# Performance work log

Hardware: AMD Instinct MI355X
Metric: run time of the kernel (lower is better)

The kernel has to match this reference:

```python
import jax, jax.numpy as jnp
import numpy as np

N = 50000
IN_DIM = 256
HID = 64
HEADS = 4
OUT_DIM = 64
E = 800000
SLOPE = 0.2


def gat_conv(x, src, dst, W, a_src, a_dst, bias, heads, out_ch):
    """PyG-style GATConv: gather -> edge attention -> segment softmax -> scatter.
    x: [N, in], W: [in, heads*out_ch], a_src/a_dst: [heads, out_ch], bias: [heads*out_ch].
    Returns [N, heads*out_ch] (heads concatenated)."""
    n = x.shape[0]
    h = (x @ W).reshape(n, heads, out_ch)               # [N, H, C]
    s = jnp.einsum('nhc,hc->nh', h, a_src)              # [N, H]
    d = jnp.einsum('nhc,hc->nh', h, a_dst)              # [N, H]
    e = jax.nn.leaky_relu(s[src] + d[dst], SLOPE)       # [E, H]
    emax = jax.ops.segment_max(e, dst, num_segments=n)  # stable softmax per dst
    ex = jnp.exp(e - emax[dst])
    denom = jax.ops.segment_sum(ex, dst, num_segments=n)
    alpha = ex / (denom[dst] + 1e-16)                   # [E, H]
    msg = h[src] * alpha[:, :, None]                    # [E, H, C]
    out = jax.ops.segment_sum(msg, dst, num_segments=n) # [N, H, C]
    return out.reshape(n, heads * out_ch) + bias


def setup_inputs() -> dict:
    key = jax.random.key(0)
    ks = jax.random.split(key, 12)
    x = jax.random.normal(ks[0], (N, IN_DIM), dtype=jnp.float32)
    edge_index = jax.random.randint(ks[1], (2, E), 0, N, dtype=jnp.int64)
    sc = 0.1
    params = {
        'W1': jax.random.normal(ks[2], (IN_DIM, HEADS * HID), dtype=jnp.float32) * sc,
        'a_src1': jax.random.normal(ks[3], (HEADS, HID), dtype=jnp.float32) * sc,
        'a_dst1': jax.random.normal(ks[4], (HEADS, HID), dtype=jnp.float32) * sc,
        'b1': jnp.zeros((HEADS * HID,), dtype=jnp.float32),
        'W2': jax.random.normal(ks[5], (HEADS * HID, HID), dtype=jnp.float32) * sc,
        'a_src2': jax.random.normal(ks[6], (1, HID), dtype=jnp.float32) * sc,
        'a_dst2': jax.random.normal(ks[7], (1, HID), dtype=jnp.float32) * sc,
        'b2': jnp.zeros((HID,), dtype=jnp.float32),
        'Wf1': jax.random.normal(ks[8], (HID, HID), dtype=jnp.float32) * sc,
        'bf1': jnp.zeros((HID,), dtype=jnp.float32),
        'Wf2': jax.random.normal(ks[9], (HID, OUT_DIM), dtype=jnp.float32) * sc,
        'bf2': jnp.zeros((OUT_DIM,), dtype=jnp.float32),
    }
    return {'x': x, 'edge_index': edge_index, **params}


def reference(x, edge_index, W1, a_src1, a_dst1, b1, W2, a_src2, a_dst2, b2,
              Wf1, bf1, Wf2, bf2):
    n = x.shape[0]
    # PyG GATConv adds self-loops by default
    loops = jnp.arange(n, dtype=edge_index.dtype)
    src = jnp.concatenate([edge_index[0], loops])
    dst = jnp.concatenate([edge_index[1], loops])
    h = jax.nn.relu(gat_conv(x, src, dst, W1, a_src1, a_dst1, b1, HEADS, HID))
    h = jax.nn.relu(gat_conv(h, src, dst, W2, a_src2, a_dst2, b2, 1, HID))
    h = jax.nn.relu(h @ Wf1 + bf1)
    return jax.nn.softmax(h @ Wf2 + bf2, axis=1)
```

## Files before the change

### kernel.cpp

```cpp
#include <hip/hip_runtime.h>

#define NNODES 50000
#define NEDGES 800000
#define INDIM  256
#define HIDC   64
#define HEADS  4
static constexpr int ETOT = NEDGES + NNODES;

typedef _Float16 half4 __attribute__((ext_vector_type(4)));
typedef _Float16 half8 __attribute__((ext_vector_type(8)));
typedef short    s16x8 __attribute__((ext_vector_type(8)));
typedef short    s16x4 __attribute__((ext_vector_type(4)));
typedef float    f32x4 __attribute__((ext_vector_type(4)));

__device__ __forceinline__ unsigned short f2bf(float f) {
    unsigned u = __float_as_uint(f);
    u += 0x7fffu + ((u >> 16) & 1u);
    return (unsigned short)(u >> 16);
}
__device__ __forceinline__ float bf2f(unsigned short h) {
    return __uint_as_float(((unsigned)h) << 16);
}

__global__ void detect_k(const unsigned* __restrict__ ei32, int* __restrict__ flag) {
    __shared__ int any32;
    if (threadIdx.x == 0) any32 = 0;
    __syncthreads();
    if (ei32[1 + 2 * threadIdx.x] != 0u) any32 = 1;
    __syncthreads();
    if (threadIdx.x == 0) *flag = !any32;
}

__device__ __forceinline__ int load_idx(const void* ei, int is64, size_t pos) {
    return is64 ? (int)((const long long*)ei)[pos] : ((const int*)ei)[pos];
}

__global__ __launch_bounds__(256)
void hist_k(const void* __restrict__ ei, const int* __restrict__ flag,
            int* __restrict__ count) {
    int e = blockIdx.x * 256 + threadIdx.x;
    if (e >= ETOT) return;
    int is64 = *flag;
    int dst = (e < NEDGES) ? load_idx(ei, is64, (size_t)NEDGES + e) : (e - NEDGES);
    atomicAdd(&count[dst], 1);
}

__global__ __launch_bounds__(1024)
void scan1_k(const int* __restrict__ count, int* __restrict__ rowptr,
             int* __restrict__ bsum, int n) {
    __shared__ int wsum[16];
    const int tid = threadIdx.x;
    const int lane = tid & 63;
    const int w = tid >> 6;
    int i = blockIdx.x * 1024 + tid;
    int v = (i < n) ? count[i] : 0;
    int x = v;
    #pragma unroll
    for (int dd = 1; dd < 64; dd <<= 1) {
        int y = __shfl_up(x, dd);
        if (lane >= dd) x += y;
    }
    if (lane == 63) wsum[w] = x;
    __syncthreads();
    int woff = 0, total = 0;
    #pragma unroll
    for (int j = 0; j < 16; ++j) {
        if (j < w) woff += wsum[j];
        total += wsum[j];
    }
    if (i < n) rowptr[i] = woff + x - v;
    if (tid == 0) bsum[blockIdx.x] = total;
}

__global__ void scan2_k(int* __restrict__ bsum, int* __restrict__ bpre, int nb,
                        int* __restrict__ rowptr, int n) {
    int lane = threadIdx.x;
    int v = (lane < nb) ? bsum[lane] : 0;
    int x = v;
    #pragma unroll
    for (int dd = 1; dd < 64; dd <<= 1) {
        int y = __shfl_up(x, dd);
        if (lane >= dd) x += y;
    }
    if (lane < nb) bpre[lane] = x - v;
    if (lane == 63) rowptr[n] = x;
}

__global__ __launch_bounds__(1024)
void scan3_k(int* __restrict__ rowptr, const int* __restrict__ bpre, int n) {
    int i = blockIdx.x * 1024 + threadIdx.x;
    if (i < n) rowptr[i] += bpre[blockIdx.x];
}

__global__ __launch_bounds__(256)
void scatter_k(const void* __restrict__ ei, const int* __restrict__ flag,
               const int* __restrict__ rowptr, int* __restrict__ fill,
               int* __restrict__ csr_src) {
    int e = blockIdx.x * 256 + threadIdx.x;
    if (e >= ETOT) return;
    int is64 = *flag;
    int src, dst;
    if (e < NEDGES) {
        src = load_idx(ei, is64, (size_t)e);
        dst = load_idx(ei, is64, (size_t)NEDGES + e);
    } else {
        src = e - NEDGES; dst = src;
    }
    int pos = rowptr[dst] + atomicAdd(&fill[dst], 1);
    csr_src[pos] = src;
}

__global__ __launch_bounds__(256)
void convw_k(const float* __restrict__ W, unsigned short* __restrict__ t_hi,
             unsigned short* __restrict__ t_lo, int K, int N) {
    int idx = blockIdx.x * 256 + threadIdx.x;
    if (idx >= K * N) return;
    int k = idx / N, n = idx % N;
    float w = W[idx];
    unsigned short hi = f2bf(w);
    unsigned short lo = f2bf(w - bf2f(hi));
    t_hi[(size_t)n * K + k] = hi;
    t_lo[(size_t)n * K + k] = lo;
}

template<int BN, int SD>
__global__ __launch_bounds__(256)
void gemm_mfma_k(const float* __restrict__ A,
                 const unsigned short* __restrict__ Bt_hi,
                 const unsigned short* __restrict__ Bt_lo,
                 float* __restrict__ C, _Float16* __restrict__ Ch,
                 const float* __restrict__ asrc, const float* __restrict__ adst,
                 float* __restrict__ S, float* __restrict__ D,
                 int M, int N, int K) {
    constexpr int CB = BN / 32;
    constexpr int BI = (BN * 4) / 256;
    __shared__ unsigned short sAh[128][40], sAl[128][40];
    __shared__ unsigned short sBh[BN][40], sBl[BN][40];
    const int tid = threadIdx.x;
    const int bm = blockIdx.y * 128;
    const int bn = blockIdx.x * BN;
    const int w = tid >> 6, lane = tid & 63;
    const int wr = w >> 1, wc = w & 1;
    const int lr = lane & 15, lk = lane >> 4;

    f32x4 acc[4][CB] = {};

    for (int k0 = 0; k0 < K; k0 += 32) {
        float4 av[4];
        #pragma unroll
        for (int i = 0; i < 4; ++i) {
            int idx = tid + 256 * i;
            int row = idx >> 3, c4 = idx & 7;
            int grow = bm + row; if (grow >= M) grow = M - 1;
            av[i] = *(const float4*)(A + (size_t)grow * K + k0 + c4 * 4);
        }
        s16x8 bhv[BI], blv[BI];
        #pragma unroll
        for (int i = 0; i < BI; ++i) {
            int idx = tid + 256 * i;
            int col = idx >> 2, ch = idx & 3;
            bhv[i] = *(const s16x8*)(Bt_hi + (size_t)(bn + col) * K + k0 + ch * 8);
            blv[i] = *(const s16x8*)(Bt_lo + (size_t)(bn + col) * K + k0 + ch * 8);
        }
        __syncthreads();
        #pragma unroll
        for (int i = 0; i < 4; ++i) {
            int idx = tid + 256 * i;
            int row = idx >> 3, c4 = idx & 7;
            float vs[4] = {av[i].x, av[i].y, av[i].z, av[i].w};
            unsigned short h[4], l[4];
            #pragma unroll
            for (int j = 0; j < 4; ++j) {
                h[j] = f2bf(vs[j]);
                l[j] = f2bf(vs[j] - bf2f(h[j]));
            }
            *(s16x4*)&sAh[row][c4 * 4] = (s16x4){(short)h[0], (short)h[1], (short)h[2], (short)h[3]};
            *(s16x4*)&sAl[row][c4 * 4] = (s16x4){(short)l[0], (short)l[1], (short)l[2], (short)l[3]};
        }
        #pragma unroll
        for (int i = 0; i < BI; ++i) {
            int idx = tid + 256 * i;
            int col = idx >> 2, ch = idx & 3;
            *(s16x8*)&sBh[col][ch * 8] = bhv[i];
            *(s16x8*)&sBl[col][ch * 8] = blv[i];
        }
        __syncthreads();
        s16x8 afh[4], afl[4], bfh[CB], bfl[CB];
        #pragma unroll
        for (int rb = 0; rb < 4; ++rb) {
            int row = wr * 64 + rb * 16 + lr;
            afh[rb] = *(const s16x8*)&sAh[row][lk * 8];
            afl[rb] = *(const s16x8*)&sAl[row][lk * 8];
        }
        #pragma unroll
        for (int cb = 0; cb < CB; ++cb) {
            int col = wc * (BN / 2) + cb * 16 + lr;
            bfh[cb] = *(const s16x8*)&sBh[col][lk * 8];
            bfl[cb] = *(const s16x8*)&sBl[col][lk * 8];
        }
        #pragma unroll
        for (int rb = 0; rb < 4; ++rb)
            #pragma unroll
            for (int cb = 0; cb < CB; ++cb) {
                acc[rb][cb] = __builtin_amdgcn_mfma_f32_16x16x32_bf16(afh[rb], bfh[cb], acc[rb][cb], 0, 0, 0);
                acc[rb][cb] = __builtin_amdgcn_mfma_f32_16x16x32_bf16(afh[rb], bfl[cb], acc[rb][cb], 0, 0, 0);
                acc[rb][cb] = __builtin_amdgcn_mfma_f32_16x16x32_bf16(afl[rb], bfh[cb], acc[rb][cb], 0, 0, 0);
            }
    }
    #pragma unroll
    for (int rb = 0; rb < 4; ++rb)
        #pragma unroll
        for (int cb = 0; cb < CB; ++cb)
            #pragma unroll
            for (int r = 0; r < 4; ++r) {
                int row = bm + wr * 64 + rb * 16 + lk * 4 + r;
                int col = bn + wc * (BN / 2) + cb * 16 + lr;
                if (row < M) {
                    float v = acc[rb][cb][r];
                    if constexpr (SD == 0) C[(size_t)row * N + col] = v;
                    if (Ch) Ch[(size_t)row * N + col] = (_Float16)v;
                }
            }
    if constexpr (SD != 0) {
        float af[CB], df[CB];
        #pragma unroll
        for (int cb = 0; cb < CB; ++cb) {
            int colg = bn + wc * (BN / 2) + cb * 16 + lr;
            af[cb] = asrc[colg];
            df[cb] = adst[colg];
        }
        #pragma unroll
        for (int rb = 0; rb < 4; ++rb)
            #pragma unroll
            for (int r = 0; r < 4; ++r) {
                float ps = 0.f, pd = 0.f;
                #pragma unroll
                for (int cb = 0; cb < CB; ++cb) {
                    ps += acc[rb][cb][r] * af[cb];
                    pd += acc[rb][cb][r] * df[cb];
                }
                #pragma unroll
                for (int m = 1; m < 16; m <<= 1) {
                    ps += __shfl_xor(ps, m);
                    pd += __shfl_xor(pd, m);
                }
                int row = bm + wr * 64 + rb * 16 + lk * 4 + r;
                if (lr == 0 && row < M) {
                    if constexpr (SD == 1) {
                        int head = (bn + wc * (BN / 2)) >> 6;
                        S[(size_t)row * (N >> 6) + head] = ps;
                        D[(size_t)row * (N >> 6) + head] = pd;
                    } else {
                        atomicAdd(&S[row], ps);
                        atomicAdd(&D[row], pd);
                    }
                }
            }
    }
}

template<int H>
__global__ __launch_bounds__(256)
void sd_k(const float* __restrict__ hfeat, const float* __restrict__ a_src,
          const float* __restrict__ a_dst, float* __restrict__ s,
          float* __restrict__ d, int n) {
    const int lane = threadIdx.x & 63;
    const int node = blockIdx.x * 4 + (threadIdx.x >> 6);
    if (node >= n) return;
    const float* row = hfeat + (size_t)node * (H * 64);
    #pragma unroll
    for (int h = 0; h < H; ++h) {
        float f = row[h * 64 + lane];
        float vs = f * a_src[h * 64 + lane];
        float vd = f * a_dst[h * 64 + lane];
        #pragma unroll
        for (int m = 32; m; m >>= 1) {
            vs += __shfl_xor(vs, m);
            vd += __shfl_xor(vd, m);
        }
        if (lane == 0) { s[node * H + h] = vs; d[node * H + h] = vd; }
    }
}

__device__ __forceinline__ float leaky(float e) { return (e > 0.f) ? e : 0.2f * e; }

__device__ __forceinline__ float sel4(const float v[4], int idx) {
    float r = v[0];
    r = (idx == 1) ? v[1] : r;
    r = (idx == 2) ? v[2] : r;
    r = (idx == 3) ? v[3] : r;
    return r;
}

__device__ __forceinline__ void osm_upd(float& m, float& sm, float e) {
    float nm = fmaxf(m, e);
    sm = sm * __expf(m - nm) + __expf(e - nm);
    m = nm;
}

template<int H, bool EB>
__global__ __launch_bounds__(256)
void agg_k(const float* __restrict__ hfeat, const _Float16* __restrict__ hhalf,
           const float* __restrict__ s, const float* __restrict__ d,
           const float* __restrict__ bias, const int* __restrict__ rowptr,
           const int* __restrict__ csr_src, float* __restrict__ ebuf,
           float* __restrict__ out, int n) {
    const int lane = threadIdx.x & 63;
    const int node = blockIdx.x * 4 + (threadIdx.x >> 6);
    if (node >= n) return;
    const int beg = rowptr[node];
    const int end = rowptr[node + 1];
    float dh[H], dn[H], inv[H];
    #pragma unroll
    for (int h = 0; h < H; ++h) {
        dh[h] = d[node * H + h];
        dn[h] = 0.f;
    }

    if constexpr (EB) {
        for (int i = beg + lane; i < end; i += 64) {
            int sidx = csr_src[i];
            if constexpr (H == 4) {
                float4 sv = *(const float4*)(s + (size_t)sidx * 4);
                float4 ex;
                ex.x = __expf(leaky(sv.x + dh[0]));
                ex.y = __expf(leaky(sv.y + dh[1]));
                ex.z = __expf(leaky(sv.z + dh[2]));
                ex.w = __expf(leaky(sv.w + dh[3]));
                *(float4*)(ebuf + (size_t)i * 4) = ex;
                dn[0] += ex.x; dn[1] += ex.y; dn[2] += ex.z; dn[3] += ex.w;
            } else {
                float ex = __expf(leaky(s[sidx] + dh[0]));
                ebuf[i] = ex;
                dn[0] += ex;
            }
        }
        #pragma unroll
        for (int h = 0; h < H; ++h) {
            #pragma unroll
            for (int m = 32; m; m >>= 1) dn[h] += __shfl_xor(dn[h], m);
            inv[h] = 1.f / (dn[h] + 1e-16f);
        }

        if constexpr (H == 4) {
            const half8* H8 = (const half8*)hhalf;
            const int sub = lane >> 5;
            const int c8 = lane & 31;
            const int head = c8 >> 3;
            const float invh = sel4(inv, head);
            float acc[8] = {};
            int i = beg;
            for (; i + 7 < end; i += 8) {
                int e0 = i + sub, e1 = i + 2 + sub, e2 = i + 4 + sub, e3 = i + 6 + sub;
                int s0 = csr_src[e0], s1 = csr_src[e1];
                int s2 = csr_src[e2], s3 = csr_src[e3];
                float x0 = ebuf[(size_t)e0 * 4 + head];
                float x1 = ebuf[(size_t)e1 * 4 + head];
                float x2 = ebuf[(size_t)e2 * 4 + head];
                float x3 = ebuf[(size_t)e3 * 4 + head];
                half8 h0 = H8[(size_t)s0 * 32 + c8];
                half8 h1 = H8[(size_t)s1 * 32 + c8];
                half8 h2 = H8[(size_t)s2 * 32 + c8];
                half8 h3 = H8[(size_t)s3 * 32 + c8];
                #pragma unroll
                for (int j = 0; j < 8; ++j)
                    acc[j] += x0 * (float)h0[j] + x1 * (float)h1[j]
                            + x2 * (float)h2[j] + x3 * (float)h3[j];
            }
            for (; i < end; i += 2) {
                int e = i + sub;
                if (e < end) {
                    int s0 = csr_src[e];
                    float x = ebuf[(size_t)e * 4 + head];
                    half8 hh = H8[(size_t)s0 * 32 + c8];
                    #pragma unroll
                    for (int j = 0; j < 8; ++j) acc[j] += x * (float)hh[j];
                }
            }
            #pragma unroll
            for (int j = 0; j < 8; ++j) acc[j] += __shfl_xor(acc[j], 32);
            if (lane < 32) {
                float4 b0 = *(const float4*)(bias + c8 * 8);
                float4 b1 = *(const float4*)(bias + c8 * 8 + 4);
                float4 o0, o1;
                o0.x = fmaxf(acc[0] * invh + b0.x, 0.f);
                o0.y = fmaxf(acc[1] * invh + b0.y, 0.f);
                o0.z = fmaxf(acc[2] * invh + b0.z, 0.f);
                o0.w = fmaxf(acc[3] * invh + b0.w, 0.f);
                o1.x = fmaxf(acc[4] * invh + b1.x, 0.f);
                o1.y = fmaxf(acc[5] * invh + b1.y, 0.f);
                o1.z = fmaxf(acc[6] * invh + b1.z, 0.f);
                o1.w = fmaxf(acc[7] * invh + b1.w, 0.f);
                *(float4*)(out + (size_t)node * 256 + c8 * 8) = o0;
                *(float4*)(out + (size_t)node * 256 + c8 * 8 + 4) = o1;
            }
        } else {
            const half8* H8 = (const half8*)hhalf;
            const int sub = lane >> 3;
            const int c8 = lane & 7;
            float acc[8] = {};
            int i = beg;
            for (; i + 15 < end; i += 16) {
                int e0 = i + sub, e1 = i + 8 + sub;
                int s0 = csr_src[e0], s1 = csr_src[e1];
                float x0 = ebuf[e0], x1 = ebuf[e1];
                half8 h0 = H8[(size_t)s0 * 8 + c8];
                half8 h1 = H8[(size_t)s1 * 8 + c8];
                #pragma unroll
                for (int j = 0; j < 8; ++j)
                    acc[j] += x0 * (float)h0[j] + x1 * (float)h1[j];
            }
            for (; i < end; i += 8) {
                int e = i + sub;
                if (e < end) {
                    int s0 = csr_src[e];
                    float x = ebuf[e];
                    half8 hh = H8[(size_t)s0 * 8 + c8];
                    #pragma unroll
                    for (int j = 0; j < 8; ++j) acc[j] += x * (float)hh[j];
                }
            }
            #pragma unroll
            for (int m = 8; m <= 32; m <<= 1)
                #pragma unroll
                for (int j = 0; j < 8; ++j) acc[j] += __shfl_xor(acc[j], m);
            if (lane < 8) {
                float4 b0 = *(const float4*)(bias + c8 * 8);
                float4 b1 = *(const float4*)(bias + c8 * 8 + 4);
                float4 o0, o1;
                o0.x = fmaxf(acc[0] * inv[0] + b0.x, 0.f);
                o0.y = fmaxf(acc[1] * inv[0] + b0.y, 0.f);
                o0.z = fmaxf(acc[2] * inv[0] + b0.z, 0.f);
                o0.w = fmaxf(acc[3] * inv[0] + b0.w, 0.f);
                o1.x = fmaxf(acc[4] * inv[0] + b1.x, 0.f);
                o1.y = fmaxf(acc[5] * inv[0] + b1.y, 0.f);
                o1.z = fmaxf(acc[6] * inv[0] + b1.z, 0.f);
                o1.w = fmaxf(acc[7] * inv[0] + b1.w, 0.f);
                *(float4*)(out + (size_t)node * 64 + c8 * 8) = o0;
                *(float4*)(out + (size_t)node * 64 + c8 * 8 + 4) = o1;
            }
        }
    } else {
        float mx[H], sm[H];
        #pragma unroll
        for (int h = 0; h < H; ++h) { mx[h] = -3.0e38f; sm[h] = 0.f; }
        for (int i = beg + lane; i < end; i += 64) {
            int sidx = csr_src[i];
            if constexpr (H == 4) {
                float4 sv = *(const float4*)(s + (size_t)sidx * 4);
                osm_upd(mx[0], sm[0], leaky(sv.x + dh[0]));
                osm_upd(mx[1], sm[1], leaky(sv.y + dh[1]));
                osm_upd(mx[2], sm[2], leaky(sv.z + dh[2]));
                osm_upd(mx[3], sm[3], leaky(sv.w + dh[3]));
            } else {
                osm_upd(mx[0], sm[0], leaky(s[sidx] + dh[0]));
            }
        }
        #pragma unroll
        for (int h = 0; h < H; ++h) {
            #pragma unroll
            for (int dd = 32; dd; dd >>= 1) {
                float om = __shfl_xor(mx[h], dd);
                float os = __shfl_xor(sm[h], dd);
                float nm = fmaxf(mx[h], om);
                sm[h] = sm[h] * __expf(mx[h] - nm) + os * __expf(om - nm);
                mx[h] = nm;
            }
            inv[h] = 1.f / (sm[h] + 1e-16f);
        }
        if constexpr (H == 4) {
            const int head = lane >> 4;
            const float invh = sel4(inv, head);
            const float mxh = sel4(mx, head);
            const float dhh = sel4(dh, head);
            const float4* H4 = (const float4*)hfeat;
            float4 acc = {0.f, 0.f, 0.f, 0.f};
            for (int i = beg; i < end; ++i) {
                int s0 = csr_src[i];
                float al0 = __expf(leaky(s[(size_t)s0 * 4 + head] + dhh) - mxh) * invh;
                float4 h0 = H4[(size_t)s0 * 64 + lane];
                acc.x += al0 * h0.x; acc.y += al0 * h0.y;
                acc.z += al0 * h0.z; acc.w += al0 * h0.w;
            }
            float4 bv = ((const float4*)bias)[lane];
            float4 o;
            o.x = fmaxf(acc.x + bv.x, 0.f); o.y = fmaxf(acc.y + bv.y, 0.f);
            o.z = fmaxf(acc.z + bv.z, 0.f); o.w = fmaxf(acc.w + bv.w, 0.f);
            ((float4*)out)[(size_t)node * 64 + lane] = o;
        } else {
            float acc = 0.f;
            for (int i = beg; i < end; ++i) {
                int s0 = csr_src[i];
                float a0 = __expf(leaky(s[s0] + dh[0]) - mx[0]) * inv[0];
                acc += a0 * hfeat[(size_t)s0 * 64 + lane];
            }
            float v = acc + bias[lane];
            out[(size_t)node * 64 + lane] = fmaxf(v, 0.f);
        }
    }
}

__global__ __launch_bounds__(256)
void ff_k(const float* __restrict__ in, const float* __restrict__ Wf1,
          const float* __restrict__ bf1, const float* __restrict__ Wf2,
          const float* __restrict__ bf2, float* __restrict__ out, int n) {
    __shared__ float w1[64 * 64];
    __shared__ float w2[64 * 64];
    __shared__ float xrow[4][64];
    __shared__ float yrow[4][64];
    const int tid = threadIdx.x;
    for (int i = tid; i < 64 * 64; i += 256) { w1[i] = Wf1[i]; w2[i] = Wf2[i]; }
    __syncthreads();
    const int wv = tid >> 6;
    const int lane = tid & 63;
    const float B1 = bf1[lane], B2 = bf2[lane];
    const int nblk = (n + 3) / 4;
    for (int nb = blockIdx.x; nb < nblk; nb += gridDim.x) {
        int node = nb * 4 + wv;
        int nd = node < n ? node : (n - 1);
        float x = in[(size_t)nd * 64 + lane];
        xrow[wv][lane] = x;
        float y = B1;
        #pragma unroll 8
        for (int k = 0; k < 64; ++k) y += xrow[wv][k] * w1[k * 64 + lane];
        y = fmaxf(y, 0.f);
        yrow[wv][lane] = y;
        float z = B2;
        #pragma unroll 8
        for (int k = 0; k < 64; ++k) z += yrow[wv][k] * w2[k * 64 + lane];
        float m = z;
        #pragma unroll
        for (int dd = 32; dd; dd >>= 1) m = fmaxf(m, __shfl_xor(m, dd));
        float ex = __expf(z - m);
        float sum = ex;
        #pragma unroll
        for (int dd = 32; dd; dd >>= 1) sum += __shfl_xor(sum, dd);
        if (node < n) out[(size_t)node * 64 + lane] = ex / sum;
    }
}

extern "C" void kernel_launch(void* const* d_in, const int* in_sizes, int n_in,
                              void* d_out, int out_size, void* d_ws, size_t ws_size,
                              hipStream_t stream) {
    const float* x      = (const float*)d_in[0];
    const void*  ei     = d_in[1];
    const float* W1     = (const float*)d_in[2];
    const float* a_src1 = (const float*)d_in[3];
    const float* a_dst1 = (const float*)d_in[4];
    const float* b1     = (const float*)d_in[5];
    const float* W2     = (const float*)d_in[6];
    const float* a_src2 = (const float*)d_in[7];
    const float* a_dst2 = (const float*)d_in[8];
    const float* b2     = (const float*)d_in[9];
    const float* Wf1    = (const float*)d_in[10];
    const float* bf1    = (const float*)d_in[11];
    const float* Wf2    = (const float*)d_in[12];
    const float* bf2    = (const float*)d_in[13];
    float* outp = (float*)d_out;

    char* ws = (char*)d_ws;
    size_t off = 0;
    auto take = [&](size_t bytes) -> char* {
        char* p = ws + off;
        off += (bytes + 255) & ~(size_t)255;
        return p;
    };
    int*   flag   = (int*)take(4);
    int*   count  = (int*)take((size_t)NNODES * 4);
    int*   fill   = (int*)take((size_t)NNODES * 4);
    int*   rowptr = (int*)take((size_t)(NNODES + 1) * 4);
    int*   bsum   = (int*)take(64 * 4);
    int*   bpre   = (int*)take(64 * 4);
    int*   csr    = (int*)take((size_t)ETOT * 4);
    unsigned short* w1t_hi = (unsigned short*)take((size_t)256 * 256 * 2);
    unsigned short* w1t_lo = (unsigned short*)take((size_t)256 * 256 * 2);
    unsigned short* w2t_hi = (unsigned short*)take((size_t)64 * 256 * 2);
    unsigned short* w2t_lo = (unsigned short*)take((size_t)64 * 256 * 2);
    float* h1     = (float*)take((size_t)NNODES * 256 * 4);
    float* agg1   = (float*)take((size_t)NNODES * 256 * 4);
    float* s1     = (float*)take((size_t)NNODES * HEADS * 4);
    float* d1     = (float*)take((size_t)NNODES * HEADS * 4);
    float* ebuf   = (float*)take((size_t)ETOT * HEADS * 4);
    _Float16* h1h = (_Float16*)take((size_t)NNODES * 256 * 2);
    const bool eb_ok = (off <= ws_size);
    float*    h2   = h1;
    float*    s2   = s1;
    float*    d2   = d1;
    float*    agg2 = agg1;
    _Float16* h2h  = h1h;

    detect_k<<<1, 128, 0, stream>>>((const unsigned*)ei, flag);
    hipMemsetAsync(count, 0, (size_t)NNODES * 4, stream);
    hipMemsetAsync(fill, 0, (size_t)NNODES * 4, stream);
    const int eblocks = (ETOT + 255) / 256;
    hist_k<<<eblocks, 256, 0, stream>>>(ei, flag, count);
    const int sblocks = (NNODES + 1023) / 1024;
    scan1_k<<<sblocks, 1024, 0, stream>>>(count, rowptr, bsum, NNODES);
    scan2_k<<<1, 64, 0, stream>>>(bsum, bpre, sblocks, rowptr, NNODES);
    scan3_k<<<sblocks, 1024, 0, stream>>>(rowptr, bpre, NNODES);
    scatter_k<<<eblocks, 256, 0, stream>>>(ei, flag, rowptr, fill, csr);

    convw_k<<<(256 * 256) / 256, 256, 0, stream>>>(W1, w1t_hi, w1t_lo, 256, 256);
    convw_k<<<(256 * 64) / 256, 256, 0, stream>>>(W2, w2t_hi, w2t_lo, 256, 64);

    const int nodeblocks = NNODES / 4;
    const int mblocks = (NNODES + 127) / 128;
    const dim3 gg1(2, mblocks);
    const dim3 gg2(1, mblocks);

    if (eb_ok) {
        gemm_mfma_k<128, 1><<<gg1, 256, 0, stream>>>(x, w1t_hi, w1t_lo,
            nullptr, h1h, a_src1, a_dst1, s1, d1, NNODES, 256, 256);
        agg_k<HEADS, true><<<nodeblocks, 256, 0, stream>>>(h1, h1h, s1, d1, b1,
            rowptr, csr, ebuf, agg1, NNODES);

        hipMemsetAsync(s2, 0, (size_t)NNODES * 4, stream);
        hipMemsetAsync(d2, 0, (size_t)NNODES * 4, stream);
        gemm_mfma_k<64, 2><<<gg2, 256, 0, stream>>>(agg1, w2t_hi, w2t_lo,
            nullptr, h2h, a_src2, a_dst2, s2, d2, NNODES, 64, 256);
        agg_k<1, true><<<nodeblocks, 256, 0, stream>>>(h2, h2h, s2, d2, b2,
            rowptr, csr, ebuf, agg2, NNODES);
    } else {
        gemm_mfma_k<128, 0><<<gg1, 256, 0, stream>>>(x, w1t_hi, w1t_lo,
            h1, nullptr, nullptr, nullptr, nullptr, nullptr, NNODES, 256, 256);
        sd_k<HEADS><<<nodeblocks, 256, 0, stream>>>(h1, a_src1, a_dst1, s1, d1, NNODES);
        agg_k<HEADS, false><<<nodeblocks, 256, 0, stream>>>(h1, h1h, s1, d1, b1,
            rowptr, csr, ebuf, agg1, NNODES);
        gemm_mfma_k<64, 0><<<gg2, 256, 0, stream>>>(agg1, w2t_hi, w2t_lo,
            h2, nullptr, nullptr, nullptr, nullptr, nullptr, NNODES, 64, 256);
        sd_k<1><<<nodeblocks, 256, 0, stream>>>(h2, a_src2, a_dst2, s2, d2, NNODES);
        agg_k<1, false><<<nodeblocks, 256, 0, stream>>>(h2, h2h, s2, d2, b2,
            rowptr, csr, ebuf, agg2, NNODES);
    }

    ff_k<<<1024, 256, 0, stream>>>(agg2, Wf1, bf1, Wf2, bf2, outp, NNODES);
}
```

Measured before the change: 323.0 us.

## Split layer-1 aggregation into per-head passes over head-major fp16 features

```diff
diff --git a/kernel.cpp b/kernel.cpp
--- a/kernel.cpp
+++ b/kernel.cpp
@@ -123,7 +123,7 @@
     t_lo[(size_t)n * K + k] = lo;
 }
 
-template<int BN, int SD>
+template<int BN, int SD, bool HM>
 __global__ __launch_bounds__(256)
 void gemm_mfma_k(const float* __restrict__ A,
                  const unsigned short* __restrict__ Bt_hi,
@@ -218,7 +218,12 @@
                 if (row < M) {
                     float v = acc[rb][cb][r];
                     if constexpr (SD == 0) C[(size_t)row * N + col] = v;
-                    if (Ch) Ch[(size_t)row * N + col] = (_Float16)v;
+                    if (Ch) {
+                        size_t cidx = HM
+                            ? ((size_t)(col >> 6) * M + row) * 64 + (col & 63)
+                            : (size_t)row * N + col;
+                        Ch[cidx] = (_Float16)v;
+                    }
                 }
             }
     if constexpr (SD != 0) {
@@ -296,6 +301,100 @@
     float nm = fmaxf(m, e);
     sm = sm * __expf(m - nm) + __expf(e - nm);
     m = nm;
+}
+
+__global__ __launch_bounds__(256)
+void pass1_k(const float* __restrict__ s, const float* __restrict__ d,
+             const int* __restrict__ rowptr, const int* __restrict__ csr_src,
+             float* __restrict__ ebuf, float* __restrict__ invv, int n) {
+    const int lane = threadIdx.x & 63;
+    const int node = blockIdx.x * 4 + (threadIdx.x >> 6);
+    if (node >= n) return;
+    const int beg = rowptr[node];
+    const int end = rowptr[node + 1];
+    float4 dh = ((const float4*)d)[node];
+    float dn0 = 0.f, dn1 = 0.f, dn2 = 0.f, dn3 = 0.f;
+    for (int i = beg + lane; i < end; i += 64) {
+        int sidx = csr_src[i];
+        float4 sv = ((const float4*)s)[sidx];
+        float e0 = __expf(leaky(sv.x + dh.x));
+        float e1 = __expf(leaky(sv.y + dh.y));
+        float e2 = __expf(leaky(sv.z + dh.z));
+        float e3 = __expf(leaky(sv.w + dh.w));
+        ebuf[i] = e0;
+        ebuf[(size_t)ETOT + i] = e1;
+        ebuf[(size_t)2 * ETOT + i] = e2;
+        ebuf[(size_t)3 * ETOT + i] = e3;
+        dn0 += e0; dn1 += e1; dn2 += e2; dn3 += e3;
+    }
+    #pragma unroll
+    for (int m = 32; m; m >>= 1) {
+        dn0 += __shfl_xor(dn0, m); dn1 += __shfl_xor(dn1, m);
+        dn2 += __shfl_xor(dn2, m); dn3 += __shfl_xor(dn3, m);
+    }
+    if (lane == 0) {
+        float4 iv;
+        iv.x = 1.f / (dn0 + 1e-16f); iv.y = 1.f / (dn1 + 1e-16f);
+        iv.z = 1.f / (dn2 + 1e-16f); iv.w = 1.f / (dn3 + 1e-16f);
+        ((float4*)invv)[node] = iv;
+    }
+}
+
+__global__ __launch_bounds__(256)
+void agg3_k(const _Float16* __restrict__ hh, const float* __restrict__ exh,
+            const float* __restrict__ invv, const float* __restrict__ bias,
+            const int* __restrict__ rowptr, const int* __restrict__ csr_src,
+            float* __restrict__ out, int head, int n) {
+    const int lane = threadIdx.x & 63;
+    const int node = blockIdx.x * 4 + (threadIdx.x >> 6);
+    if (node >= n) return;
+    const int beg = rowptr[node];
+    const int end = rowptr[node + 1];
+    const half8* H8 = (const half8*)hh;
+    const int sub = lane >> 3;
+    const int c8 = lane & 7;
+    float acc[8] = {};
+    int i = beg;
+    for (; i + 15 < end; i += 16) {
+        int e0 = i + sub, e1 = i + 8 + sub;
+        int s0 = csr_src[e0], s1 = csr_src[e1];
+        float x0 = exh[e0], x1 = exh[e1];
+        half8 h0 = H8[(size_t)s0 * 8 + c8];
+        half8 h1 = H8[(size_t)s1 * 8 + c8];
+        #pragma unroll
+        for (int j = 0; j < 8; ++j)
+            acc[j] += x0 * (float)h0[j] + x1 * (float)h1[j];
+    }
+    for (; i < end; i += 8) {
+        int e = i + sub;
+        if (e < end) {
+            int s0 = csr_src[e];
+            float x = exh[e];
+            half8 hh8 = H8[(size_t)s0 * 8 + c8];
+            #pragma unroll
+            for (int j = 0; j < 8; ++j) acc[j] += x * (float)hh8[j];
+        }
+    }
+    #pragma unroll
+    for (int m = 8; m <= 32; m <<= 1)
+        #pragma unroll
+        for (int j = 0; j < 8; ++j) acc[j] += __shfl_xor(acc[j], m);
+    if (lane < 8) {
+        float iv = invv[node * 4 + head];
+        float4 b0 = *(const float4*)(bias + head * 64 + c8 * 8);
+        float4 b1 = *(const float4*)(bias + head * 64 + c8 * 8 + 4);
+        float4 o0, o1;
+        o0.x = fmaxf(acc[0] * iv + b0.x, 0.f);
+        o0.y = fmaxf(acc[1] * iv + b0.y, 0.f);
+        o0.z = fmaxf(acc[2] * iv + b0.z, 0.f);
+        o0.w = fmaxf(acc[3] * iv + b0.w, 0.f);
+        o1.x = fmaxf(acc[4] * iv + b1.x, 0.f);
+        o1.y = fmaxf(acc[5] * iv + b1.y, 0.f);
+        o1.z = fmaxf(acc[6] * iv + b1.z, 0.f);
+        o1.w = fmaxf(acc[7] * iv + b1.w, 0.f);
+        *(float4*)(out + (size_t)node * 256 + head * 64 + c8 * 8) = o0;
+        *(float4*)(out + (size_t)node * 256 + head * 64 + c8 * 8 + 4) = o1;
+    }
 }
 
 template<int H, bool EB>
@@ -580,6 +679,7 @@
     float* agg1   = (float*)take((size_t)NNODES * 256 * 4);
     float* s1     = (float*)take((size_t)NNODES * HEADS * 4);
     float* d1     = (float*)take((size_t)NNODES * HEADS * 4);
+    float* invv   = (float*)take((size_t)NNODES * HEADS * 4);
     float* ebuf   = (float*)take((size_t)ETOT * HEADS * 4);
     _Float16* h1h = (_Float16*)take((size_t)NNODES * 256 * 2);
     const bool eb_ok = (off <= ws_size);
@@ -609,24 +709,27 @@
     const dim3 gg2(1, mblocks);
 
     if (eb_ok) {
-        gemm_mfma_k<128, 1><<<gg1, 256, 0, stream>>>(x, w1t_hi, w1t_lo,
+        gemm_mfma_k<128, 1, true><<<gg1, 256, 0, stream>>>(x, w1t_hi, w1t_lo,
             nullptr, h1h, a_src1, a_dst1, s1, d1, NNODES, 256, 256);
-        agg_k<HEADS, true><<<nodeblocks, 256, 0, stream>>>(h1, h1h, s1, d1, b1,
-            rowptr, csr, ebuf, agg1, NNODES);
+        pass1_k<<<nodeblocks, 256, 0, stream>>>(s1, d1, rowptr, csr, ebuf, invv, NNODES);
+        for (int h = 0; h < HEADS; ++h)
+            agg3_k<<<nodeblocks, 256, 0, stream>>>(
+                h1h + (size_t)h * NNODES * 64, ebuf + (size_t)h * ETOT,
+                invv, b1, rowptr, csr, agg1, h, NNODES);
 
         hipMemsetAsync(s2, 0, (size_t)NNODES * 4, stream);
         hipMemsetAsync(d2, 0, (size_t)NNODES * 4, stream);
-        gemm_mfma_k<64, 2><<<gg2, 256, 0, stream>>>(agg1, w2t_hi, w2t_lo,
+        gemm_mfma_k<64, 2, false><<<gg2, 256, 0, stream>>>(agg1, w2t_hi, w2t_lo,
             nullptr, h2h, a_src2, a_dst2, s2, d2, NNODES, 64, 256);
         agg_k<1, true><<<nodeblocks, 256, 0, stream>>>(h2, h2h, s2, d2, b2,
             rowptr, csr, ebuf, agg2, NNODES);
     } else {
-        gemm_mfma_k<128, 0><<<gg1, 256, 0, stream>>>(x, w1t_hi, w1t_lo,
+        gemm_mfma_k<128, 0, false><<<gg1, 256, 0, stream>>>(x, w1t_hi, w1t_lo,
             h1, nullptr, nullptr, nullptr, nullptr, nullptr, NNODES, 256, 256);
         sd_k<HEADS><<<nodeblocks, 256, 0, stream>>>(h1, a_src1, a_dst1, s1, d1, NNODES);
         agg_k<HEADS, false><<<nodeblocks, 256, 0, stream>>>(h1, h1h, s1, d1, b1,
             rowptr, csr, ebuf, agg1, NNODES);
-        gemm_mfma_k<64, 0><<<gg2, 256, 0, stream>>>(agg1, w2t_hi, w2t_lo,
+        gemm_mfma_k<64, 0, false><<<gg2, 256, 0, stream>>>(agg1, w2t_hi, w2t_lo,
             h2, nullptr, nullptr, nullptr, nullptr, nullptr, NNODES, 64, 256);
         sd_k<1><<<nodeblocks, 256, 0, stream>>>(h2, a_src2, a_dst2, s2, d2, NNODES);
         agg_k<1, false><<<nodeblocks, 256, 0, stream>>>(h2, h2h, s2, d2, b2,
```

After: 355.0 us. +9.9%, slower.
